# Kernel tuning notes

Measured on AMD Instinct MI355X. Metric: run time of the kernel, lower is better.

Reference implementation:

```python
import jax, jax.numpy as jnp
import numpy as np

POOL = 14  # pool_size from __init__


def setup_inputs() -> dict:
    key = jax.random.key(0)
    k1, k2, k3, k4 = jax.random.split(key, 4)
    B, H, W, C, N = 2, 128, 128, 256, 512
    features = jax.random.normal(k1, (B, H, W, C), dtype=jnp.float32)
    # roi layout per original code: [y1, x1, y2, x2]; crop = features[img, x1:x2, y1:y2, :]
    y1 = jax.random.randint(k2, (B, N, 1), 0, H - 16)
    x1 = jax.random.randint(k3, (B, N, 1), 0, W - 16)
    hw = jax.random.randint(k4, (B, N, 2), 8, 16)  # box sizes in [8,16)
    roi = jnp.concatenate([y1, x1, y1 + hw[..., :1], x1 + hw[..., 1:]], axis=-1).astype(jnp.int32)
    return {"features": features, "roi": roi}


def _legacy_resize_axis(start, end, pool):
    """Legacy TF1 bilinear resize (align_corners=False): local src coord = i * (size/pool).
    Returns global low/high integer indices and interpolation fractions, shapes [R, pool]."""
    size = (end - start).astype(jnp.float32)  # [R]
    local = jnp.arange(pool, dtype=jnp.float32)[None, :] * size[:, None] / pool  # [R,P]
    i0 = jnp.floor(local).astype(jnp.int32)
    i1 = jnp.minimum(i0 + 1, (end - start - 1)[:, None])  # clamp inside the crop
    frac = local - i0.astype(jnp.float32)
    return start[:, None] + i0, start[:, None] + i1, frac


def reference(features, roi):
    B, H, W, C = features.shape
    N = roi.shape[1]
    pool = POOL
    roi = roi.reshape(-1, 4)  # [R,4] rows of (y1, x1, y2, x2), R = B*N
    img = jnp.repeat(jnp.arange(B, dtype=jnp.int32), N)  # image index per ROI, [R]
    y1, x1, y2, x2 = roi[:, 0], roi[:, 1], roi[:, 2], roi[:, 3]
    # Original slices rows with x1:x2 and cols with y1:y2; crop+resize == direct
    # bilinear sampling in the full map at global coords start + i*size/pool.
    r0, r1, fr = _legacy_resize_axis(x1, x2, pool)  # rows,   [R,P]
    c0, c1, fc = _legacy_resize_axis(y1, y2, pool)  # cols,   [R,P]

    def gather(r, c):
        # [R,P,P,C] fused gather over all ROIs at once (replaces tf.scan)
        return features[img[:, None, None], r[:, :, None], c[:, None, :], :]

    fr = fr[:, :, None, None]
    fc = fc[:, None, :, None]
    top = gather(r0, c0) * (1.0 - fc) + gather(r0, c1) * fc
    bot = gather(r1, c0) * (1.0 - fc) + gather(r1, c1) * fc
    return top * (1.0 - fr) + bot * fr  # [B*N, pool, pool, C]
```

## Files before the change

### kernel.cpp

```cpp
#include <hip/hip_runtime.h>


typedef float f32x4 __attribute__((ext_vector_type(4)));

#define NROI 1024
#define CMAX 15
#define THREADS 448
#define NWG (NROI * 14)
#define WG_PER_XCD (NWG / 8)

__global__ __launch_bounds__(THREADS) void rpn_pool_kernel(
    const float* __restrict__ feat,
    const int*   __restrict__ roi,
    float*       __restrict__ out)
{
    __shared__ float lds[2][CMAX][256];

    const int d = blockIdx.x;
    const int w = (d & 7) * WG_PER_XCD + (d >> 3);
    const int q = w / 14;
    const int i = w - q * 14;
    const int b = q >> 9;

    const int4 rr = ((const int4*)roi)[q];
    const int y1 = rr.x, x1 = rr.y, y2 = rr.z, x2 = rr.w;

    const int sR = x2 - x1;
    const int sC = y2 - y1;

    const int pr  = i * sR;
    const int ir0 = pr / 14;
    const float fr = (float)(pr - ir0 * 14) * (1.0f / 14.0f);
    const int r0 = x1 + ir0;
    const int r1 = x1 + min(ir0 + 1, sR - 1);

    const size_t SB = (size_t)128 * 128 * 256;
    const size_t SR = (size_t)128 * 256;

    const float* base = feat + (size_t)b * SB;
    const f32x4* row0 = (const f32x4*)(base + (size_t)r0 * SR + (size_t)y1 * 256);
    const f32x4* row1 = (const f32x4*)(base + (size_t)r1 * SR + (size_t)y1 * 256);

    const int rowElems = sC * 64;
    f32x4* lds4 = (f32x4*)lds;
    for (int idx = threadIdx.x; idx < rowElems; idx += THREADS)
        lds4[idx] = row0[idx];
    for (int idx = threadIdx.x; idx < rowElems; idx += THREADS)
        lds4[CMAX * 64 + idx] = row1[idx];
    __syncthreads();

    const int wave = threadIdx.x >> 6;
    const int lane = threadIdx.x & 63;
    const float wr1 = 1.0f - fr;

    for (int j = wave; j < 14; j += 7) {
        const int pc  = j * sC;
        const int ic0 = pc / 14;
        const float fc = (float)(pc - ic0 * 14) * (1.0f / 14.0f);
        const int c0 = ic0;
        const int c1 = min(ic0 + 1, sC - 1);
        const float wc1 = 1.0f - fc;

        const f32x4 g00 = ((const f32x4*)lds[0][c0])[lane];
        const f32x4 g01 = ((const f32x4*)lds[0][c1])[lane];
        const f32x4 g10 = ((const f32x4*)lds[1][c0])[lane];
        const f32x4 g11 = ((const f32x4*)lds[1][c1])[lane];

        f32x4 o = (g00 * wc1 + g01 * fc) * wr1 + (g10 * wc1 + g11 * fc) * fr;

        const size_t oidx = ((size_t)q * 196 + (size_t)i * 14 + j) * 64 + lane;
        __builtin_nontemporal_store(o, ((f32x4*)out) + oidx);
    }
}

extern "C" void kernel_launch(void* const* d_in, const int* in_sizes, int n_in,
                              void* d_out, int out_size, void* d_ws, size_t ws_size,
                              hipStream_t stream) {
    const float* feat = (const float*)d_in[0];
    const int*   roi  = (const int*)d_in[1];
    float* out = (float*)d_out;

    rpn_pool_kernel<<<NWG, THREADS, 0, stream>>>(feat, roi, out);
}
```

Baseline: 53.52 us.

## Sort ROIs by Morton-coded spatial position to improve feature cache locality

```diff
diff --git a/kernel.cpp b/kernel.cpp
--- a/kernel.cpp
+++ b/kernel.cpp
@@ -9,17 +9,49 @@
 #define NWG (NROI * 14)
 #define WG_PER_XCD (NWG / 8)
 
+__device__ __forceinline__ unsigned spread3(unsigned v) {
+    v &= 7u;
+    return (v & 1u) | ((v & 2u) << 1) | ((v & 4u) << 2);
+}
+
+__global__ __launch_bounds__(1024) void roi_sort_kernel(
+    const int* __restrict__ roi, int* __restrict__ perm)
+{
+    __shared__ unsigned key[NROI];
+    const int t = threadIdx.x;
+    const int4 rr = ((const int4*)roi)[t];
+    const int b = t >> 9;
+    const unsigned m = spread3((unsigned)rr.y >> 4) | (spread3((unsigned)rr.x >> 4) << 1);
+    key[t] = ((((unsigned)b << 6) | m) << 10) | (unsigned)t;
+    __syncthreads();
+    for (int size = 2; size <= NROI; size <<= 1) {
+        for (int stride = size >> 1; stride > 0; stride >>= 1) {
+            const int p = t ^ stride;
+            const unsigned a  = key[t];
+            const unsigned bk = key[p];
+            __syncthreads();
+            const bool asc = ((t & size) == 0);
+            const bool keepmin = ((t < p) == asc);
+            key[t] = keepmin ? min(a, bk) : max(a, bk);
+            __syncthreads();
+        }
+    }
+    perm[t] = (int)(key[t] & 1023u);
+}
+
 __global__ __launch_bounds__(THREADS) void rpn_pool_kernel(
     const float* __restrict__ feat,
     const int*   __restrict__ roi,
+    const int*   __restrict__ perm,
     float*       __restrict__ out)
 {
     __shared__ float lds[2][CMAX][256];
 
     const int d = blockIdx.x;
     const int w = (d & 7) * WG_PER_XCD + (d >> 3);
-    const int q = w / 14;
-    const int i = w - q * 14;
+    const int g = w / 14;
+    const int i = w - g * 14;
+    const int q = perm[g];
     const int b = q >> 9;
 
     const int4 rr = ((const int4*)roi)[q];
@@ -79,6 +111,8 @@
     const float* feat = (const float*)d_in[0];
     const int*   roi  = (const int*)d_in[1];
     float* out = (float*)d_out;
+    int*   perm = (int*)d_ws;
 
-    rpn_pool_kernel<<<NWG, THREADS, 0, stream>>>(feat, roi, out);
+    roi_sort_kernel<<<1, 1024, 0, stream>>>(roi, perm);
+    rpn_pool_kernel<<<NWG, THREADS, 0, stream>>>(feat, roi, perm, out);
 }
```

After: 54.32 us. Within noise of the previous version (+1.5%).

## Process one ROI per workgroup with a rolling three-row LDS buffer

Applied to the files above, without the earlier changes.

```diff
diff --git a/kernel.cpp b/kernel.cpp
--- a/kernel.cpp
+++ b/kernel.cpp
@@ -5,71 +5,87 @@
 
 #define NROI 1024
 #define CMAX 15
-#define THREADS 448
-#define NWG (NROI * 14)
-#define WG_PER_XCD (NWG / 8)
+#define THREADS 896
 
 __global__ __launch_bounds__(THREADS) void rpn_pool_kernel(
     const float* __restrict__ feat,
     const int*   __restrict__ roi,
     float*       __restrict__ out)
 {
-    __shared__ float lds[2][CMAX][256];
+    __shared__ f32x4 lds[3][CMAX * 64];
 
     const int d = blockIdx.x;
-    const int w = (d & 7) * WG_PER_XCD + (d >> 3);
-    const int q = w / 14;
-    const int i = w - q * 14;
+    const int q = (d & 7) * (NROI / 8) + (d >> 3);
     const int b = q >> 9;
 
     const int4 rr = ((const int4*)roi)[q];
     const int y1 = rr.x, x1 = rr.y, y2 = rr.z, x2 = rr.w;
-
     const int sR = x2 - x1;
     const int sC = y2 - y1;
-
-    const int pr  = i * sR;
-    const int ir0 = pr / 14;
-    const float fr = (float)(pr - ir0 * 14) * (1.0f / 14.0f);
-    const int r0 = x1 + ir0;
-    const int r1 = x1 + min(ir0 + 1, sR - 1);
+    const int rowElems = sC * 64;
 
     const size_t SB = (size_t)128 * 128 * 256;
     const size_t SR = (size_t)128 * 256;
+    const float* base = feat + (size_t)b * SB + (size_t)x1 * SR + (size_t)y1 * 256;
 
-    const float* base = feat + (size_t)b * SB;
-    const f32x4* row0 = (const f32x4*)(base + (size_t)r0 * SR + (size_t)y1 * 256);
-    const f32x4* row1 = (const f32x4*)(base + (size_t)r1 * SR + (size_t)y1 * 256);
+    const int t    = threadIdx.x;
+    const int wave = t >> 6;
+    const int lane = t & 63;
 
-    const int rowElems = sC * 64;
-    f32x4* lds4 = (f32x4*)lds;
-    for (int idx = threadIdx.x; idx < rowElems; idx += THREADS)
-        lds4[idx] = row0[idx];
-    for (int idx = threadIdx.x; idx < rowElems; idx += THREADS)
-        lds4[CMAX * 64 + idx] = row1[idx];
+    {
+        const f32x4* r0p = (const f32x4*)base;
+        const f32x4* r1p = (const f32x4*)(base + SR);
+        if (t < rowElems)           { lds[0][t] = r0p[t];  lds[1][t] = r1p[t]; }
+        if (t + THREADS < rowElems) { lds[0][t + THREADS] = r0p[t + THREADS];
+                                      lds[1][t + THREADS] = r1p[t + THREADS]; }
+    }
     __syncthreads();
+    int hi = 1;
 
-    const int wave = threadIdx.x >> 6;
-    const int lane = threadIdx.x & 63;
-    const float wr1 = 1.0f - fr;
+    const int j   = wave;
+    const int pc  = j * sC;
+    const int ic0 = pc / 14;
+    const float fc  = (float)(pc - ic0 * 14) * (1.0f / 14.0f);
+    const float wc1 = 1.0f - fc;
+    const int c0 = ic0 * 64 + lane;
+    const int c1 = min(ic0 + 1, sC - 1) * 64 + lane;
 
-    for (int j = wave; j < 14; j += 7) {
-        const int pc  = j * sC;
-        const int ic0 = pc / 14;
-        const float fc = (float)(pc - ic0 * 14) * (1.0f / 14.0f);
-        const int c0 = ic0;
-        const int c1 = min(ic0 + 1, sC - 1);
-        const float wc1 = 1.0f - fc;
+    for (int i = 0; i < 14; ++i) {
+        const int pr  = i * sR;
+        const int ir0 = pr / 14;
+        const float fr = (float)(pr - ir0 * 14) * (1.0f / 14.0f);
+        const int rA = ir0;
+        const int rB = min(ir0 + 1, sR - 1);
 
-        const f32x4 g00 = ((const f32x4*)lds[0][c0])[lane];
-        const f32x4 g01 = ((const f32x4*)lds[0][c1])[lane];
-        const f32x4 g10 = ((const f32x4*)lds[1][c0])[lane];
-        const f32x4 g11 = ((const f32x4*)lds[1][c1])[lane];
+        int nextHi = hi;
+        f32x4 v0, v1;
+        bool ld0 = false, ld1 = false;
+        if (i < 13) {
+            const int need = min((i + 1) * sR / 14 + 1, sR - 1);
+            if (need > hi) {
+                nextHi = hi + 1;
+                const f32x4* rp = (const f32x4*)(base + (size_t)nextHi * SR);
+                if (t < rowElems)           { v0 = rp[t];           ld0 = true; }
+                if (t + THREADS < rowElems) { v1 = rp[t + THREADS]; ld1 = true; }
+            }
+        }
 
-        f32x4 o = (g00 * wc1 + g01 * fc) * wr1 + (g10 * wc1 + g11 * fc) * fr;
-
+        const int sA = rA % 3, sB = rB % 3;
+        const f32x4 g00 = lds[sA][c0];
+        const f32x4 g01 = lds[sA][c1];
+        const f32x4 g10 = lds[sB][c0];
+        const f32x4 g11 = lds[sB][c1];
+        f32x4 o = (g00 * wc1 + g01 * fc) * (1.0f - fr) + (g10 * wc1 + g11 * fc) * fr;
         const size_t oidx = ((size_t)q * 196 + (size_t)i * 14 + j) * 64 + lane;
         __builtin_nontemporal_store(o, ((f32x4*)out) + oidx);
+
+        if (nextHi != hi) {
+            const int slot = nextHi % 3;
+            if (ld0) lds[slot][t] = v0;
+            if (ld1) lds[slot][t + THREADS] = v1;
+            hi = nextHi;
+        }
+        __syncthreads();
     }
 }
 
@@ -80,5 +96,5 @@
     const int*   roi  = (const int*)d_in[1];
     float* out = (float*)d_out;
 
-    rpn_pool_kernel<<<NWG, THREADS, 0, stream>>>(feat, roi, out);
+    rpn_pool_kernel<<<NROI, THREADS, 0, stream>>>(feat, roi, out);
 }
```

Result: faster. 50.92 us (-4.9%).

## Assign one wave per output column and slide row registers instead of LDS staging

Applied to the files above, without the earlier changes.

```diff
diff --git a/kernel.cpp b/kernel.cpp
--- a/kernel.cpp
+++ b/kernel.cpp
@@ -4,72 +4,74 @@
 typedef float f32x4 __attribute__((ext_vector_type(4)));
 
 #define NROI 1024
-#define CMAX 15
-#define THREADS 448
-#define NWG (NROI * 14)
-#define WG_PER_XCD (NWG / 8)
+#define WAVES_TOTAL (NROI * 14)
+#define THREADS 256
+#define NBLK (WAVES_TOTAL / 4)
 
 __global__ __launch_bounds__(THREADS) void rpn_pool_kernel(
     const float* __restrict__ feat,
     const int*   __restrict__ roi,
     float*       __restrict__ out)
 {
-    __shared__ float lds[2][CMAX][256];
+    const int lane = threadIdx.x & 63;
+    const int wv   = threadIdx.x >> 6;
 
-    const int d = blockIdx.x;
-    const int w = (d & 7) * WG_PER_XCD + (d >> 3);
-    const int q = w / 14;
-    const int i = w - q * 14;
-    const int b = q >> 9;
+    const int d   = blockIdx.x;
+    const int blk = (d & 7) * (NBLK / 8) + (d >> 3);
+    const int W   = blk * 4 + wv;
+    const int q   = W / 14;
+    const int j   = W - q * 14;
+    const int b   = q >> 9;
 
     const int4 rr = ((const int4*)roi)[q];
     const int y1 = rr.x, x1 = rr.y, y2 = rr.z, x2 = rr.w;
-
     const int sR = x2 - x1;
     const int sC = y2 - y1;
 
-    const int pr  = i * sR;
-    const int ir0 = pr / 14;
-    const float fr = (float)(pr - ir0 * 14) * (1.0f / 14.0f);
-    const int r0 = x1 + ir0;
-    const int r1 = x1 + min(ir0 + 1, sR - 1);
+    const int pc  = j * sC;
+    const int ic0 = pc / 14;
+    const float fc  = (float)(pc - ic0 * 14) * (1.0f / 14.0f);
+    const float wc1 = 1.0f - fc;
+    const int c0 = ic0;
+    const int c1 = min(ic0 + 1, sC - 1);
 
-    const size_t SB = (size_t)128 * 128 * 256;
-    const size_t SR = (size_t)128 * 256;
+    const size_t SB4 = (size_t)128 * 128 * 64;
+    const size_t SR4 = (size_t)128 * 64;
+    const f32x4* base = (const f32x4*)feat + (size_t)b * SB4
+                        + (size_t)x1 * SR4 + (size_t)y1 * 64 + lane;
+    const size_t o0 = (size_t)c0 * 64, o1 = (size_t)c1 * 64;
 
-    const float* base = feat + (size_t)b * SB;
-    const f32x4* row0 = (const f32x4*)(base + (size_t)r0 * SR + (size_t)y1 * 256);
-    const f32x4* row1 = (const f32x4*)(base + (size_t)r1 * SR + (size_t)y1 * 256);
+    int rA = 0, rB = min(1, sR - 1);
+    f32x4 a0 = base[o0];
+    f32x4 a1 = base[o1];
+    f32x4 b0 = base[(size_t)rB * SR4 + o0];
+    f32x4 b1 = base[(size_t)rB * SR4 + o1];
 
-    const int rowElems = sC * 64;
-    f32x4* lds4 = (f32x4*)lds;
-    for (int idx = threadIdx.x; idx < rowElems; idx += THREADS)
-        lds4[idx] = row0[idx];
-    for (int idx = threadIdx.x; idx < rowElems; idx += THREADS)
-        lds4[CMAX * 64 + idx] = row1[idx];
-    __syncthreads();
+    f32x4* outp = (f32x4*)out + ((size_t)q * 196 + j) * 64 + lane;
 
-    const int wave = threadIdx.x >> 6;
-    const int lane = threadIdx.x & 63;
-    const float wr1 = 1.0f - fr;
+    for (int i = 0; i < 14; ++i) {
+        const int pr = i * sR;
+        const float fr = (float)(pr - rA * 14) * (1.0f / 14.0f);
 
-    for (int j = wave; j < 14; j += 7) {
-        const int pc  = j * sC;
-        const int ic0 = pc / 14;
-        const float fc = (float)(pc - ic0 * 14) * (1.0f / 14.0f);
-        const int c0 = ic0;
-        const int c1 = min(ic0 + 1, sC - 1);
-        const float wc1 = 1.0f - fc;
+        int nA = rA, nB = rB;
+        f32x4 p0, p1;
+        bool adv = false;
+        if (i < 13) {
+            nA = ((i + 1) * sR) / 14;
+            nB = min(nA + 1, sR - 1);
+            if (nB > rB) {
+                p0 = base[(size_t)nB * SR4 + o0];
+                p1 = base[(size_t)nB * SR4 + o1];
+                adv = true;
+            }
+        }
 
-        const f32x4 g00 = ((const f32x4*)lds[0][c0])[lane];
-        const f32x4 g01 = ((const f32x4*)lds[0][c1])[lane];
-        const f32x4 g10 = ((const f32x4*)lds[1][c0])[lane];
-        const f32x4 g11 = ((const f32x4*)lds[1][c1])[lane];
+        f32x4 o = (a0 * wc1 + a1 * fc) * (1.0f - fr) + (b0 * wc1 + b1 * fc) * fr;
+        __builtin_nontemporal_store(o, outp + (size_t)i * 14 * 64);
 
-        f32x4 o = (g00 * wc1 + g01 * fc) * wr1 + (g10 * wc1 + g11 * fc) * fr;
-
-        const size_t oidx = ((size_t)q * 196 + (size_t)i * 14 + j) * 64 + lane;
-        __builtin_nontemporal_store(o, ((f32x4*)out) + oidx);
+        if (nA > rA) { a0 = b0; a1 = b1; }
+        if (adv)     { b0 = p0; b1 = p1; }
+        rA = nA; rB = nB;
     }
 }
 
@@ -80,5 +82,5 @@
     const int*   roi  = (const int*)d_in[1];
     float* out = (float*)d_out;
 
-    rpn_pool_kernel<<<NWG, THREADS, 0, stream>>>(feat, roi, out);
+    rpn_pool_kernel<<<NBLK, THREADS, 0, stream>>>(feat, roi, out);
 }
```

After: 51.11 us. 4.5% less time.
